# Kernel optimization log

Measured on AMD Instinct MI355X. Metric: run time of the kernel, lower is better.

The kernel has to match this reference:

```python
import jax, jax.numpy as jnp
import numpy as np

K1, K2, K3 = 36, 36, 2  # rolled-patch sizes hardcoded in unfolding()


def _patch_indices(C, H, W, k1=K1, k2=K2, k3=K3):
    """Precompute gather indices replacing the triple-nested torch.roll loops.

    Column col=(k*k2+j)*k1+i of Ak_3D holds X rolled by (k,i,j) along (C,H,W):
      A[b, c*H*W+h*W+w, col] = X[b, (c-k)%C, (h-i)%H, (w-j)%W]
    The adjoint gathers with +k,+i,+j shifts.
    """
    Kc = k1 * k2 * k3
    col = np.arange(Kc)
    kk = col // (k1 * k2)
    jj = (col % (k1 * k2)) // k1
    ii = col % k1
    cg, hg, wg = np.meshgrid(np.arange(C), np.arange(H), np.arange(W), indexing='ij')
    cg = cg.reshape(-1, 1); hg = hg.reshape(-1, 1); wg = wg.reshape(-1, 1)
    fwd = ((cg - kk) % C) * (H * W) + ((hg - ii) % H) * W + ((wg - jj) % W)
    adj = ((cg + kk) % C) * (H * W) + ((hg + ii) % H) * W + ((wg + jj) % W)
    return jnp.asarray(fwd, jnp.int32), jnp.asarray(adj, jnp.int32)


def _unfold(input_img, S0, alpha, beta, gamma, iters):
    B, C, H, W = input_img.shape
    m = C * H * W
    mk = (H * W) // 64
    Kc = K1 * K2 * K3
    fwd_idx, adj_idx = _patch_indices(C, H, W)
    colr = jnp.arange(Kc, dtype=jnp.int32)

    def Ak(x):  # [B,C,H,W] -> [B, m, Kc] (single gather == Ak_3D)
        return x.reshape(B, m)[:, fwd_idx]

    def Ak_adj(A):  # [B, m, Kc] -> [B,C,H,W] (== Ak_adj_3D)
        g = A[:, adj_idx, colr[None, :]]  # [B, m, Kc]
        return (g.sum(-1) / Kc).reshape(B, C, H, W)

    a3 = alpha[:, None, None]
    g3 = gamma[:, None, None]
    g4 = gamma[:, None, None, None]
    b4 = beta[:, None, None, None]
    I_mk = jnp.eye(mk, dtype=input_img.dtype)

    # t == 0 initialization (L detached, S random-clamped from setup, M/N rect. identities)
    L0 = jax.lax.stop_gradient(input_img)
    M0 = jnp.broadcast_to(jnp.eye(m, mk, dtype=input_img.dtype), (B, m, mk))
    N0 = jnp.broadcast_to(jnp.eye(mk, Kc, dtype=input_img.dtype), (B, mk, Kc))

    def step(carry, _):
        Lc, Sc, Mc, Nc = carry
        MN = Mc @ Nc                                        # [B, m, Kc]
        Ln = jnp.clip((input_img - Sc + g4 * Ak_adj(MN)) / (g4 + 1.0), 0.0, 1.0)
        Sn = (input_img - Ln) / (b4 + 1.0)
        AkL = Ak(Ln)                                        # [B, m, Kc]
        # M-update: 2g * Ak_L N^T pinv(a I + 2g N N^T)
        Cm = a3 * I_mk + 2.0 * g3 * (Nc @ Nc.transpose(0, 2, 1))      # [B, mk, mk]
        Mn = 2.0 * g3 * ((AkL @ Nc.transpose(0, 2, 1)) @ jnp.linalg.pinv(Cm))
        # N-update: 2g * pinv(a I + 2g M^T M) M^T Ak_L
        Cn = a3 * I_mk + 2.0 * g3 * (Mn.transpose(0, 2, 1) @ Mn)      # [B, mk, mk]
        Nn = 2.0 * g3 * (jnp.linalg.pinv(Cn) @ (Mn.transpose(0, 2, 1) @ AkL))
        return (Ln, Sn, Mn, Nn), None

    (Lf, _, _, _), _ = jax.lax.scan(step, (L0, S0, M0, N0), None, length=iters - 1)
    return Lf


def setup_inputs() -> dict:
    key = jax.random.key(0)
    k1, k2 = jax.random.split(key)
    B, C, H, W = 1, 2, 64, 64
    input_img = jax.random.uniform(k1, (B, C, H, W), jnp.float32)
    S0 = jnp.clip(jax.random.normal(k2, (B, C, H, W), jnp.float32), 0.0, 1.0)  # clamp(randn_like,0,1)
    alpha = jnp.full((B,), 10.0, jnp.float32)  # w_alpha
    beta = jnp.full((B,), 2.0, jnp.float32)    # w_beta
    gamma = jnp.full((B,), 10.0, jnp.float32)  # w_gamma
    return {"input_img": input_img, "S0": S0, "alpha": alpha, "beta": beta,
            "gamma": gamma, "iters": 6}


def reference(input_img, S0, alpha, beta, gamma, iters):
    return _unfold(input_img, S0, alpha, beta, gamma, iters)
```

## Files before the change

### kernel.cpp

```cpp
#include <hip/hip_runtime.h>

#define KC 2592
#define KCP 2624
#define HW 4096

#define OFF_L    0u
#define OFF_S    8192u
#define OFF_MT   16384u
#define OFF_NTT  540672u
#define OFF_BIG  708608u
#define OFF_GRAM 2805760u
#define OFF_CMI  2809856u
#define OFF_CNI  2813952u
#define OFF_ST   2818048u

__global__ __launch_bounds__(256) void k_init(const float* __restrict__ inp, const float* __restrict__ s0,
                                              float* __restrict__ L, float* __restrict__ S,
                                              float* __restrict__ Mt, float* __restrict__ NtT){
  int t = blockIdx.x * 256 + threadIdx.x;
  if (t < 8192){ L[t] = inp[t]; S[t] = s0[t]; }
  if (t < 524288){ int r = t >> 13; int p = t & 8191; Mt[t] = (p == r) ? 1.0f : 0.0f; }
  if (t < 167936){ int r = t / KCP; int d = t - r * KCP;
                   int dr = (r % 36) * 36 + r / 36;
                   NtT[t] = (d == dr) ? 1.0f : 0.0f; }
}

__device__ __forceinline__ float readlane_f(float x, int lane){
  return __uint_as_float(__builtin_amdgcn_readlane(__float_as_uint(x), lane));
}
template<int K>
__device__ __forceinline__ void gj_step(float (&b)[64], int lane){
  float bk = b[K];
  float akk = readlane_f(bk, K);
  float p = 1.0f / akk;
  bool isk = (lane == K);
  float t = isk ? 1.0f : bk;
  float pt = p * t;
  #pragma unroll
  for (int g = 0; g < 4; g++){
    float f[16];
    #pragma unroll
    for (int u = 0; u < 16; u++){
      int i = g * 16 + u;
      if (i == K) continue;
      f[u] = readlane_f(b[i], K);
    }
    #pragma unroll
    for (int u = 0; u < 16; u++){
      int i = g * 16 + u;
      if (i == K) continue;
      float base = isk ? 0.0f : b[i];
      b[i] = fmaf(-f[u], pt, base);
    }
  }
  b[K] = t * p;
}
template<int K0, int K1> struct GJR {
  static __device__ __forceinline__ void run(float (&b)[64], int lane){
    gj_step<K0>(b, lane);
    GJR<K0 + 1, K1>::run(b, lane);
  }
};
template<int KE> struct GJR<KE, KE> {
  static __device__ __forceinline__ void run(float (&b)[64], int lane){}
};
template<int PH>
__device__ void inv64_phaseA(const float* __restrict__ src, const float* __restrict__ pg,
                             const float* __restrict__ pa, float* __restrict__ state, int lane){
  float scale = 2.0f * pg[0];
  float ad = pa[0];
  float b[64];
  #pragma unroll
  for (int i = 0; i < 64; i++)
    b[i] = scale * src[i * 64 + lane] + ((i == lane) ? ad : 0.0f);
  GJR<0, PH>::run(b, lane);
  #pragma unroll
  for (int i = 0; i < 64; i++) state[i * 64 + lane] = b[i];
}
template<int PH>
__device__ void inv64_phaseB(const float* __restrict__ state, float* __restrict__ dst, int lane){
  float b[64];
  #pragma unroll
  for (int i = 0; i < 64; i++) b[i] = state[i * 64 + lane];
  GJR<PH, 64>::run(b, lane);
  #pragma unroll
  for (int i = 0; i < 64; i++) dst[i * 64 + lane] = b[i];
}

__global__ __launch_bounds__(64) void k_conv_R(const float* __restrict__ Mtg,
                                               const float* __restrict__ NtT,
                                               float* __restrict__ Rpart,
                                               const float* __restrict__ Gr,
                                               const float* __restrict__ pg,
                                               const float* __restrict__ pa,
                                               float* __restrict__ state){
  __shared__ float img[2][16][68];
  __shared__ float4 filt4[162];
  if (blockIdx.z == 4){
    if (blockIdx.x == 0 && blockIdx.y == 0)
      inv64_phaseA<32>(Gr, pg, pa, state, threadIdx.x);
    return;
  }
  int r = blockIdx.x, oct = blockIdx.y, z = blockIdx.z, tid = threadIdx.x;
  int rowbase = oct * 8 + z * 9;
  const float4* gi4 = (const float4*)(Mtg + (size_t)r * 8192);
  for (int t = tid; t < 512; t += 64){
    int fw = t & 15, rr = t >> 4;
    int c = rr >> 4, q = rr & 15;
    int gr = (rowbase + q) & 63;
    float4 v4 = gi4[(c * 64 + gr) * 16 + fw];
    float* d = &img[c][q][fw * 4];
    d[0] = v4.x; d[1] = v4.y; d[2] = v4.z; d[3] = v4.w;
  }
  int iilo = z * 9;
  const float* gf = NtT + (size_t)r * KCP;
  for (int t = tid; t < 162; t += 64){
    int kk = t / 81; int rem4 = t - kk * 81;
    filt4[t] = *(const float4*)(gf + kk * 1296 + iilo * 36 + rem4 * 4);
  }
  __syncthreads();
  int c0 = tid >> 5, hl = (tid >> 2) & 7, w0 = (tid & 3) * 16;
  float acc[16];
  #pragma unroll
  for (int u = 0; u < 16; u++) acc[u] = 0.0f;
  #pragma unroll 1
  for (int kk = 0; kk < 2; kk++){
    int cimg = (c0 + kk) & 1;
    #pragma unroll 1
    for (int iix = 0; iix < 9; iix++){
      const float* ib = img[cimg][hl + iix];
      float v[32];
      #pragma unroll
      for (int t = 0; t < 8; t++){
        float4 t4 = *(const float4*)&ib[(w0 + 4 * t) & 63];
        v[4*t] = t4.x; v[4*t+1] = t4.y; v[4*t+2] = t4.z; v[4*t+3] = t4.w;
      }
      const float4* fb = &filt4[kk * 81 + iix * 9];
      #pragma unroll
      for (int g = 0; g < 9; g++){
        float4 ff = fb[g];
        #pragma unroll
        for (int u = 0; u < 16; u++) acc[u] = fmaf(ff.x, v[(4*g + 0 + u) & 31], acc[u]);
        #pragma unroll
        for (int u = 0; u < 16; u++) acc[u] = fmaf(ff.y, v[(4*g + 1 + u) & 31], acc[u]);
        #pragma unroll
        for (int u = 0; u < 16; u++) acc[u] = fmaf(ff.z, v[(4*g + 2 + u) & 31], acc[u]);
        #pragma unroll
        for (int u = 0; u < 16; u++) acc[u] = fmaf(ff.w, v[(4*g + 3 + u) & 31], acc[u]);
        if (g < 5){
          float4 nv = *(const float4*)&ib[(w0 + 32 + 4*g) & 63];
          int s = (4*g) & 31;
          v[s] = nv.x; v[s+1] = nv.y; v[s+2] = nv.z; v[s+3] = nv.w;
        }
      }
    }
  }
  int h = oct * 8 + hl;
  size_t ob = ((size_t)r + 64 * z) * 8192 + (size_t)(c0 * HW + h * 64 + w0);
  *(float4*)&Rpart[ob]      = make_float4(acc[0], acc[1], acc[2], acc[3]);
  *(float4*)&Rpart[ob + 4]  = make_float4(acc[4], acc[5], acc[6], acc[7]);
  *(float4*)&Rpart[ob + 8]  = make_float4(acc[8], acc[9], acc[10], acc[11]);
  *(float4*)&Rpart[ob + 12] = make_float4(acc[12], acc[13], acc[14], acc[15]);
}

__global__ __launch_bounds__(64) void k_conv_T1(const float* __restrict__ Lg,
                                                const float* __restrict__ NtT,
                                                float* __restrict__ T1t,
                                                const float* __restrict__ state,
                                                float* __restrict__ CmI){
  __shared__ float img[2][16][68];
  __shared__ float4 filt4[162];
  if (blockIdx.z == 4){
    if (blockIdx.x == 0 && blockIdx.y == 0)
      inv64_phaseB<32>(state, CmI, threadIdx.x);
    return;
  }
  int r = blockIdx.x, oct = blockIdx.y, z = blockIdx.z, tid = threadIdx.x;
  int rowbase = (oct * 8 - z * 9 - 8 + 128) & 63;
  const float4* gi4 = (const float4*)Lg;
  for (int t = tid; t < 512; t += 64){
    int fw = t & 15, rr = t >> 4;
    int c = rr >> 4, q = rr & 15;
    int gr = (rowbase + q) & 63;
    float4 v4 = gi4[(c * 64 + gr) * 16 + fw];
    float* d = &img[c][q][fw * 4];
    d[0] = v4.x; d[1] = v4.y; d[2] = v4.z; d[3] = v4.w;
  }
  int iilo = z * 9;
  const float* gf = NtT + (size_t)r * KCP;
  for (int t = tid; t < 162; t += 64){
    int kk = t / 81; int rem4 = t - kk * 81;
    filt4[t] = *(const float4*)(gf + kk * 1296 + iilo * 36 + rem4 * 4);
  }
  __syncthreads();
  int c0 = tid >> 5, hl = (tid >> 2) & 7, w0 = (tid & 3) * 16;
  float acc[16];
  #pragma unroll
  for (int u = 0; u < 16; u++) acc[u] = 0.0f;
  #pragma unroll 1
  for (int kk = 0; kk < 2; kk++){
    int cimg = (c0 - kk + 2) & 1;
    #pragma unroll 1
    for (int iix = 0; iix < 9; iix++){
      const float* ib = img[cimg][hl - iix + 8];
      float v[32];
      {
        float4 tm = *(const float4*)&ib[(w0 - 4 + 64) & 63];
        v[28] = tm.x; v[29] = tm.y; v[30] = tm.z; v[31] = tm.w;
      }
      #pragma unroll
      for (int t = 0; t < 4; t++){
        float4 t4 = *(const float4*)&ib[(w0 + 4 * t) & 63];
        v[4*t] = t4.x; v[4*t+1] = t4.y; v[4*t+2] = t4.z; v[4*t+3] = t4.w;
      }
      const float4* fb = &filt4[kk * 81 + iix * 9];
      #pragma unroll
      for (int g = 0; g < 9; g++){
        float4 ff = fb[g];
        #pragma unroll
        for (int u = 0; u < 16; u++) acc[u] = fmaf(ff.x, v[(u - (4*g + 0)) & 31], acc[u]);
        #pragma unroll
        for (int u = 0; u < 16; u++) acc[u] = fmaf(ff.y, v[(u - (4*g + 1)) & 31], acc[u]);
        #pragma unroll
        for (int u = 0; u < 16; u++) acc[u] = fmaf(ff.z, v[(u - (4*g + 2)) & 31], acc[u]);
        #pragma unroll
        for (int u = 0; u < 16; u++) acc[u] = fmaf(ff.w, v[(u - (4*g + 3)) & 31], acc[u]);
        if (g < 8){
          float4 nv = *(const float4*)&ib[(w0 - 8 - 4*g + 128) & 63];
          int s = (-8 - 4*g) & 31;
          v[s] = nv.x; v[s+1] = nv.y; v[s+2] = nv.z; v[s+3] = nv.w;
        }
      }
    }
  }
  int h = oct * 8 + hl;
  size_t ob = ((size_t)r + 64 * z) * 8192 + (size_t)(c0 * HW + h * 64 + w0);
  *(float4*)&T1t[ob]      = make_float4(acc[0], acc[1], acc[2], acc[3]);
  *(float4*)&T1t[ob + 4]  = make_float4(acc[4], acc[5], acc[6], acc[7]);
  *(float4*)&T1t[ob + 8]  = make_float4(acc[8], acc[9], acc[10], acc[11]);
  *(float4*)&T1t[ob + 12] = make_float4(acc[12], acc[13], acc[14], acc[15]);
}

__global__ __launch_bounds__(256) void k_reduce_LS(const float* __restrict__ Rpart,
                                                   const float* __restrict__ inp,
                                                   const float* __restrict__ pg, const float* __restrict__ pb,
                                                   float* __restrict__ S, float* __restrict__ Ldst){
  __shared__ float red[8][32];
  int tid = threadIdx.x;
  int pi = tid & 31, sg = tid >> 5;
  int p = blockIdx.x * 32 + pi;
  float acc = 0.0f;
  #pragma unroll 4
  for (int s = sg * 32; s < sg * 32 + 32; s++) acc += Rpart[(size_t)s * 8192 + p];
  red[sg][pi] = acc;
  __syncthreads();
  if (tid < 32){
    float a = 0.0f;
    #pragma unroll
    for (int q = 0; q < 8; q++) a += red[q][pi];
    float R = a * (1.0f / 2592.0f);
    float g = pg[0], b = pb[0];
    float Ln = (inp[p] - S[p] + g * R) / (g + 1.0f);
    Ln = fminf(fmaxf(Ln, 0.0f), 1.0f);
    S[p] = (inp[p] - Ln) / (b + 1.0f);
    Ldst[p] = Ln;
  }
}

__global__ __launch_bounds__(64) void k_gram(const float* __restrict__ rows, int stride, int len4,
                                             float* __restrict__ out){
  int e = blockIdx.x; int r1 = e >> 6, r2 = e & 63;
  if (r2 < r1) return;
  int lane = threadIdx.x;
  const float4* a = (const float4*)(rows + (size_t)r1 * stride);
  const float4* b = (const float4*)(rows + (size_t)r2 * stride);
  float acc = 0.0f;
  for (int p = lane; p < len4; p += 64){
    float4 x = a[p], y = b[p];
    acc = fmaf(x.x, y.x, acc); acc = fmaf(x.y, y.y, acc);
    acc = fmaf(x.z, y.z, acc); acc = fmaf(x.w, y.w, acc);
  }
  for (int off = 32; off; off >>= 1) acc += __shfl_down(acc, off, 64);
  if (lane == 0){ out[r1 * 64 + r2] = acc; out[r2 * 64 + r1] = acc; }
}

__global__ __launch_bounds__(256) void k_mn(const float* __restrict__ T1t, const float* __restrict__ CmInv,
                                            const float* __restrict__ pg, float* __restrict__ Mt){
  __shared__ float4 ci4[1024];
  int tid = threadIdx.x;
  const float4* g4 = (const float4*)CmInv;
  for (int t = tid; t < 1024; t += 256) ci4[t] = g4[t];
  __syncthreads();
  int p = blockIdx.x * 256 + tid;
  int sbase = blockIdx.y * 32;
  float g2 = 2.0f * pg[0];
  float acc[32];
  #pragma unroll
  for (int s = 0; s < 32; s++) acc[s] = 0.0f;
  for (int r = 0; r < 64; r++){
    float v = T1t[(size_t)r * 8192 + p] + T1t[(size_t)(r + 64) * 8192 + p]
            + T1t[(size_t)(r + 128) * 8192 + p] + T1t[(size_t)(r + 192) * 8192 + p];
    #pragma unroll
    for (int k = 0; k < 8; k++){
      float4 c = ci4[r * 16 + (sbase >> 2) + k];
      acc[4*k+0] = fmaf(v, c.x, acc[4*k+0]);
      acc[4*k+1] = fmaf(v, c.y, acc[4*k+1]);
      acc[4*k+2] = fmaf(v, c.z, acc[4*k+2]);
      acc[4*k+3] = fmaf(v, c.w, acc[4*k+3]);
    }
  }
  #pragma unroll
  for (int s = 0; s < 32; s++) Mt[(size_t)(sbase + s) * 8192 + p] = g2 * acc[s];
}

__global__ __launch_bounds__(256) void k_conv_T2(const float* __restrict__ Lg,
                                                 const float* __restrict__ Mtg,
                                                 float* __restrict__ T2part,
                                                 const float* __restrict__ Gr,
                                                 const float* __restrict__ pg,
                                                 const float* __restrict__ pa,
                                                 float* __restrict__ state){
  __shared__ float Mi[128 * 68];
  __shared__ float4 Ls4[256];
  if (blockIdx.y == 8){
    if (blockIdx.x == 0 && threadIdx.x < 64)
      inv64_phaseA<48>(Gr, pg, pa, state, threadIdx.x);
    return;
  }
  int r = blockIdx.x, hc = blockIdx.y, tid = threadIdx.x;
  const float4* gm4 = (const float4*)(Mtg + (size_t)r * 8192);
  for (int t = tid; t < 2048; t += 256){
    float4 v4 = gm4[t];
    int row = t >> 4, cb = (t & 15) * 4;
    float* d = &Mi[row * 68 + cb];
    d[0] = v4.x; d[1] = v4.y; d[2] = v4.z; d[3] = v4.w;
  }
  const float4* gl4 = (const float4*)Lg;
  if (tid < 256){
    int c = tid >> 7, rem = tid & 127;
    Ls4[tid] = gl4[c * 1024 + hc * 128 + rem];
  }
  __syncthreads();
  if (tid >= 216) return;
  int kk = tid / 108, rest = tid % 108, ii = rest / 3, jj0 = (rest % 3) * 12;
  float acc[12];
  #pragma unroll
  for (int u = 0; u < 12; u++) acc[u] = 0.0f;
  #pragma unroll 1
  for (int c = 0; c < 2; c++){
    #pragma unroll 1
    for (int hl = 0; hl < 8; hl++){
      int h = hc * 8 + hl;
      const float* ib = &Mi[(((c + kk) & 1) * 64 + ((h + ii) & 63)) * 68];
      const float4* lrow = &Ls4[c * 128 + hl * 16];
      float v[16];
      {
        float4 t0 = *(const float4*)&ib[jj0];
        float4 t1 = *(const float4*)&ib[jj0 + 4];
        float4 t2 = *(const float4*)&ib[jj0 + 8];
        float4 t3 = *(const float4*)&ib[jj0 + 12];
        v[0]=t0.x; v[1]=t0.y; v[2]=t0.z; v[3]=t0.w;
        v[4]=t1.x; v[5]=t1.y; v[6]=t1.z; v[7]=t1.w;
        v[8]=t2.x; v[9]=t2.y; v[10]=t2.z; v[11]=t2.w;
        v[12]=t3.x; v[13]=t3.y; v[14]=t3.z; v[15]=t3.w;
      }
      #pragma unroll
      for (int wg = 0; wg < 16; wg++){
        float4 lv = lrow[wg];
        #pragma unroll
        for (int u = 0; u < 12; u++) acc[u] = fmaf(lv.x, v[(4*wg + 0 + u) & 15], acc[u]);
        #pragma unroll
        for (int u = 0; u < 12; u++) acc[u] = fmaf(lv.y, v[(4*wg + 1 + u) & 15], acc[u]);
        #pragma unroll
        for (int u = 0; u < 12; u++) acc[u] = fmaf(lv.z, v[(4*wg + 2 + u) & 15], acc[u]);
        #pragma unroll
        for (int u = 0; u < 12; u++) acc[u] = fmaf(lv.w, v[(4*wg + 3 + u) & 15], acc[u]);
        if (wg < 15){
          float4 nv = *(const float4*)&ib[(jj0 + 4*wg + 16) & 63];
          int s = (4*wg) & 15;
          v[s] = nv.x; v[s+1] = nv.y; v[s+2] = nv.z; v[s+3] = nv.w;
        }
      }
    }
  }
  #pragma unroll
  for (int u = 0; u < 12; u++){
    int col = kk * 1296 + (jj0 + u) * 36 + ii;
    T2part[((size_t)hc * 64 + r) * KC + col] = acc[u];
  }
}

__global__ __launch_bounds__(256) void k_t2sum(const float* __restrict__ T2part, float* __restrict__ T2sum,
                                               const float* __restrict__ state, float* __restrict__ CnI){
  if (blockIdx.x == 648){
    if (threadIdx.x < 64)
      inv64_phaseB<48>(state, CnI, threadIdx.x);
    return;
  }
  int t = blockIdx.x * 256 + threadIdx.x;
  float s = 0.0f;
  #pragma unroll
  for (int hc = 0; hc < 8; hc++) s += T2part[(size_t)hc * 165888 + t];
  T2sum[t] = s;
}

__global__ __launch_bounds__(256) void k_nn(const float* __restrict__ T2sum, const float* __restrict__ CnInv,
                                            const float* __restrict__ pg,
                                            float* __restrict__ NtT){
  __shared__ float4 ci4[1024];
  int tid = threadIdx.x;
  const float4* g4 = (const float4*)CnInv;
  for (int t = tid; t < 1024; t += 256) ci4[t] = g4[t];
  __syncthreads();
  int col = blockIdx.x * 256 + tid;
  if (col >= KC) return;
  int rb = blockIdx.y * 16;
  float g2 = 2.0f * pg[0];
  float acc[16];
  #pragma unroll
  for (int rr = 0; rr < 16; rr++) acc[rr] = 0.0f;
  for (int s = 0; s < 64; s++){
    float tv = T2sum[(size_t)s * KC + col];
    #pragma unroll
    for (int k = 0; k < 4; k++){
      float4 c = ci4[s * 16 + (rb >> 2) + k];
      acc[4*k+0] = fmaf(tv, c.x, acc[4*k+0]);
      acc[4*k+1] = fmaf(tv, c.y, acc[4*k+1]);
      acc[4*k+2] = fmaf(tv, c.z, acc[4*k+2]);
      acc[4*k+3] = fmaf(tv, c.w, acc[4*k+3]);
    }
  }
  int kk = col / 1296, rest = col % 1296, jj = rest / 36, iv = rest % 36;
  int d = (kk * 36 + iv) * 36 + jj;
  #pragma unroll
  for (int rr = 0; rr < 16; rr++){
    NtT[(size_t)(rb + rr) * KCP + d] = g2 * acc[rr];
  }
}

extern "C" void kernel_launch(void* const* d_in, const int* in_sizes, int n_in,
                              void* d_out, int out_size, void* d_ws, size_t ws_size,
                              hipStream_t stream) {
  const float* inp = (const float*)d_in[0];
  const float* s0  = (const float*)d_in[1];
  const float* pa  = (const float*)d_in[2];
  const float* pb  = (const float*)d_in[3];
  const float* pg  = (const float*)d_in[4];
  float* ws  = (float*)d_ws;
  float* L   = ws + OFF_L;   float* S   = ws + OFF_S;    float* Mt  = ws + OFF_MT;
  float* NtT = ws + OFF_NTT; float* Big = ws + OFF_BIG;
  float* T2p = ws + OFF_BIG;
  float* T2s = ws + OFF_BIG + 1327104u;
  float* Gr  = ws + OFF_GRAM;
  float* CmI = ws + OFF_CMI; float* CnI = ws + OFF_CNI;
  float* St  = ws + OFF_ST;
  float* out = (float*)d_out;

  k_init<<<2048, 256, 0, stream>>>(inp, s0, L, S, Mt, NtT);
  for (int step = 0; step < 5; step++){
    bool last = (step == 4);
    if (!last)
      k_gram<<<4096, 64, 0, stream>>>(NtT, KCP, KCP / 4, Gr);
    k_conv_R<<<dim3(64, 8, last ? 4 : 5), 64, 0, stream>>>(Mt, NtT, Big, Gr, pg, pa, St);
    k_reduce_LS<<<256, 256, 0, stream>>>(Big, inp, pg, pb, S, last ? out : L);
    if (last) break;
    k_conv_T1<<<dim3(64, 8, 5), 64, 0, stream>>>(L, NtT, Big, St, CmI);
    k_mn<<<dim3(32, 2), 256, 0, stream>>>(Big, CmI, pg, Mt);
    k_gram<<<4096, 64, 0, stream>>>(Mt, 8192, 2048, Gr);
    k_conv_T2<<<dim3(64, 9), 256, 0, stream>>>(L, Mt, T2p, Gr, pg, pa, St);
    k_t2sum<<<649, 256, 0, stream>>>(T2p, T2s, St, CnI);
    k_nn<<<dim3(11, 4), 256, 0, stream>>>(T2s, CnI, pg, NtT);
  }
}
```

Baseline: 886.2 us.

## Fuse T2 partial reduction into conv kernel via atomics, drop t2sum kernel

The T2 convolution now splits the image into 16 row chunks of 4, stages only the 39 needed rows of M per channel in shared memory, and accumulates straight into T2sum with atomicAdd. The separate partial-sum kernel goes away, and the 64x64 Cn inverse now runs in one block instead of two phases. T2sum is zeroed by the idle lower-triangle blocks of k_gram, which launches before the conv. This removes one kernel launch and the 8x partial buffer round-trip, at the cost of atomic contention, nondeterministic summation order, and a longer serial inverse inside one block.

```diff
diff --git a/kernel.cpp b/kernel.cpp
--- a/kernel.cpp
+++ b/kernel.cpp
@@ -83,6 +83,18 @@
   #pragma unroll
   for (int i = 0; i < 64; i++) b[i] = state[i * 64 + lane];
   GJR<PH, 64>::run(b, lane);
+  #pragma unroll
+  for (int i = 0; i < 64; i++) dst[i * 64 + lane] = b[i];
+}
+__device__ void inv64_full(const float* __restrict__ src, const float* __restrict__ pg,
+                           const float* __restrict__ pa, float* __restrict__ dst, int lane){
+  float scale = 2.0f * pg[0];
+  float ad = pa[0];
+  float b[64];
+  #pragma unroll
+  for (int i = 0; i < 64; i++)
+    b[i] = scale * src[i * 64 + lane] + ((i == lane) ? ad : 0.0f);
+  GJR<0, 64>::run(b, lane);
   #pragma unroll
   for (int i = 0; i < 64; i++) dst[i * 64 + lane] = b[i];
 }
@@ -268,10 +280,15 @@
 }
 
 __global__ __launch_bounds__(64) void k_gram(const float* __restrict__ rows, int stride, int len4,
-                                             float* __restrict__ out){
+                                             float* __restrict__ out, float* __restrict__ zt){
   int e = blockIdx.x; int r1 = e >> 6, r2 = e & 63;
-  if (r2 < r1) return;
   int lane = threadIdx.x;
+  if (r2 < r1){
+    int idx = (r1 * (r1 - 1)) / 2 + r2;
+    int t = idx * 64 + lane;
+    if (t < 41472) ((float4*)zt)[t] = make_float4(0.f, 0.f, 0.f, 0.f);
+    return;
+  }
   const float4* a = (const float4*)(rows + (size_t)r1 * stride);
   const float4* b = (const float4*)(rows + (size_t)r2 * stride);
   float acc = 0.0f;
@@ -315,30 +332,33 @@
 
 __global__ __launch_bounds__(256) void k_conv_T2(const float* __restrict__ Lg,
                                                  const float* __restrict__ Mtg,
-                                                 float* __restrict__ T2part,
+                                                 float* __restrict__ T2sum,
                                                  const float* __restrict__ Gr,
                                                  const float* __restrict__ pg,
                                                  const float* __restrict__ pa,
-                                                 float* __restrict__ state){
-  __shared__ float Mi[128 * 68];
-  __shared__ float4 Ls4[256];
-  if (blockIdx.y == 8){
+                                                 float* __restrict__ CnI){
+  __shared__ float Mi[2 * 39 * 68];
+  __shared__ float4 Ls4[128];
+  if (blockIdx.y == 16){
     if (blockIdx.x == 0 && threadIdx.x < 64)
-      inv64_phaseA<48>(Gr, pg, pa, state, threadIdx.x);
+      inv64_full(Gr, pg, pa, CnI, threadIdx.x);
     return;
   }
-  int r = blockIdx.x, hc = blockIdx.y, tid = threadIdx.x;
+  int r = blockIdx.x, hcc = blockIdx.y, tid = threadIdx.x;
+  int h0 = hcc * 4;
   const float4* gm4 = (const float4*)(Mtg + (size_t)r * 8192);
-  for (int t = tid; t < 2048; t += 256){
-    float4 v4 = gm4[t];
-    int row = t >> 4, cb = (t & 15) * 4;
-    float* d = &Mi[row * 68 + cb];
+  for (int t = tid; t < 1248; t += 256){
+    int fw = t & 15, rr = t >> 4;
+    int c = (rr >= 39) ? 1 : 0, q = rr - c * 39;
+    int gr = (h0 + q) & 63;
+    float4 v4 = gm4[(c * 64 + gr) * 16 + fw];
+    float* d = &Mi[(c * 39 + q) * 68 + fw * 4];
     d[0] = v4.x; d[1] = v4.y; d[2] = v4.z; d[3] = v4.w;
   }
   const float4* gl4 = (const float4*)Lg;
-  if (tid < 256){
-    int c = tid >> 7, rem = tid & 127;
-    Ls4[tid] = gl4[c * 1024 + hc * 128 + rem];
+  if (tid < 128){
+    int c = tid >> 6, rem = tid & 63;
+    Ls4[tid] = gl4[c * 1024 + (h0 + (rem >> 4)) * 16 + (rem & 15)];
   }
   __syncthreads();
   if (tid >= 216) return;
@@ -348,11 +368,11 @@
   for (int u = 0; u < 12; u++) acc[u] = 0.0f;
   #pragma unroll 1
   for (int c = 0; c < 2; c++){
+    int cimg = (c + kk) & 1;
     #pragma unroll 1
-    for (int hl = 0; hl < 8; hl++){
-      int h = hc * 8 + hl;
-      const float* ib = &Mi[(((c + kk) & 1) * 64 + ((h + ii) & 63)) * 68];
-      const float4* lrow = &Ls4[c * 128 + hl * 16];
+    for (int hl = 0; hl < 4; hl++){
+      const float* ib = &Mi[(cimg * 39 + hl + ii) * 68];
+      const float4* lrow = &Ls4[c * 64 + hl * 16];
       float v[16];
       {
         float4 t0 = *(const float4*)&ib[jj0];
@@ -386,22 +406,8 @@
   #pragma unroll
   for (int u = 0; u < 12; u++){
     int col = kk * 1296 + (jj0 + u) * 36 + ii;
-    T2part[((size_t)hc * 64 + r) * KC + col] = acc[u];
-  }
-}
-
-__global__ __launch_bounds__(256) void k_t2sum(const float* __restrict__ T2part, float* __restrict__ T2sum,
-                                               const float* __restrict__ state, float* __restrict__ CnI){
-  if (blockIdx.x == 648){
-    if (threadIdx.x < 64)
-      inv64_phaseB<48>(state, CnI, threadIdx.x);
-    return;
-  }
-  int t = blockIdx.x * 256 + threadIdx.x;
-  float s = 0.0f;
-  #pragma unroll
-  for (int hc = 0; hc < 8; hc++) s += T2part[(size_t)hc * 165888 + t];
-  T2sum[t] = s;
+    atomicAdd(&T2sum[(size_t)r * KC + col], acc[u]);
+  }
 }
 
 __global__ __launch_bounds__(256) void k_nn(const float* __restrict__ T2sum, const float* __restrict__ CnInv,
@@ -449,7 +455,6 @@
   float* ws  = (float*)d_ws;
   float* L   = ws + OFF_L;   float* S   = ws + OFF_S;    float* Mt  = ws + OFF_MT;
   float* NtT = ws + OFF_NTT; float* Big = ws + OFF_BIG;
-  float* T2p = ws + OFF_BIG;
   float* T2s = ws + OFF_BIG + 1327104u;
   float* Gr  = ws + OFF_GRAM;
   float* CmI = ws + OFF_CMI; float* CnI = ws + OFF_CNI;
@@ -460,15 +465,14 @@
   for (int step = 0; step < 5; step++){
     bool last = (step == 4);
     if (!last)
-      k_gram<<<4096, 64, 0, stream>>>(NtT, KCP, KCP / 4, Gr);
+      k_gram<<<4096, 64, 0, stream>>>(NtT, KCP, KCP / 4, Gr, T2s);
     k_conv_R<<<dim3(64, 8, last ? 4 : 5), 64, 0, stream>>>(Mt, NtT, Big, Gr, pg, pa, St);
     k_reduce_LS<<<256, 256, 0, stream>>>(Big, inp, pg, pb, S, last ? out : L);
     if (last) break;
     k_conv_T1<<<dim3(64, 8, 5), 64, 0, stream>>>(L, NtT, Big, St, CmI);
     k_mn<<<dim3(32, 2), 256, 0, stream>>>(Big, CmI, pg, Mt);
-    k_gram<<<4096, 64, 0, stream>>>(Mt, 8192, 2048, Gr);
-    k_conv_T2<<<dim3(64, 9), 256, 0, stream>>>(L, Mt, T2p, Gr, pg, pa, St);
-    k_t2sum<<<649, 256, 0, stream>>>(T2p, T2s, St, CnI);
+    k_gram<<<4096, 64, 0, stream>>>(Mt, 8192, 2048, Gr, T2s);
+    k_conv_T2<<<dim3(64, 17), 256, 0, stream>>>(L, Mt, T2s, Gr, pg, pa, CnI);
     k_nn<<<dim3(11, 4), 256, 0, stream>>>(T2s, CnI, pg, NtT);
   }
 }
```

Result: slower. 949.3 us (+7.1%).
